# Kernel optimization log

Hardware: AMD Instinct MI355X
Metric: run time of the kernel (lower is better)

Reference implementation:

```python
import jax, jax.numpy as jnp
import numpy as np

EPS_NORM = 1e-12  # F.normalize eps
LN_EPS = 1e-5


def _ln(x, g, b):
    mu = x.mean(-1, keepdims=True)
    var = ((x - mu) ** 2).mean(-1, keepdims=True)
    return (x - mu) / jnp.sqrt(var + LN_EPS) * g + b


def _gate(x, w1, b1, g, b, w2, b2):
    # Linear -> LayerNorm(32) -> SiLU -> Linear -> Sigmoid, squeeze(-1)
    t = _ln(x @ w1 + b1, g, b)
    t = jax.nn.silu(t)
    return jax.nn.sigmoid(t @ w2 + b2)[..., 0]


def setup_inputs() -> dict:
    key = jax.random.key(0)
    B, N, D, dH, S, HID = 4, 4096, 1024, 256, 256, 32
    ks = jax.random.split(key, 24)
    sc_d = 0.5 * (6.0 / (D + dH)) ** 0.5  # xavier gain=0.5 approx
    sc_h = 0.5 * (6.0 / (D + HID)) ** 0.5
    inp = {
        "h": jax.random.normal(ks[0], (B, N, D), jnp.float32),
        # encoder complex projection (stored as (in,out))
        "Wr": jax.random.uniform(ks[1], (D, dH), jnp.float32, -sc_d, sc_d),
        "br": jnp.zeros((dH,), jnp.float32),
        "Wi": jax.random.uniform(ks[2], (D, dH), jnp.float32, -sc_d, sc_d),
        "bi": jnp.zeros((dH,), jnp.float32),
        # uncertainty net
        "uw1": jax.random.uniform(ks[3], (D, HID), jnp.float32, -sc_h, sc_h),
        "ub1": jnp.zeros((HID,), jnp.float32),
        "ug": jnp.ones((HID,), jnp.float32),
        "ubeta": jnp.zeros((HID,), jnp.float32),
        "uw2": jax.random.uniform(ks[4], (HID, 1), jnp.float32, -0.2, 0.2),
        "ub2": jnp.zeros((1,), jnp.float32),
        # decoherence gamma net
        "gw1": jax.random.uniform(ks[5], (D, HID), jnp.float32, -sc_h, sc_h),
        "gb1": jnp.zeros((HID,), jnp.float32),
        "gg": jnp.ones((HID,), jnp.float32),
        "gbeta": jnp.zeros((HID,), jnp.float32),
        "gw2": jax.random.uniform(ks[6], (HID, 1), jnp.float32, -0.2, 0.2),
        "gb2": jnp.zeros((1,), jnp.float32),
        # memory attention params
        "m_real": jax.random.normal(ks[7], (S, dH), jnp.float32) / dH ** 0.5,
        "m_imag": jax.random.normal(ks[8], (S, dH), jnp.float32) / dH ** 0.5,
        "values": jax.random.normal(ks[9], (S, D), jnp.float32) * 0.02,
        "ow": jax.random.uniform(ks[10], (D, D), jnp.float32, -0.5 * (3.0 / D) ** 0.5, 0.5 * (3.0 / D) ** 0.5),
        "ob": jnp.zeros((D,), jnp.float32),
        # norms
        "n1g": jnp.ones((D,), jnp.float32),
        "n1b": jnp.zeros((D,), jnp.float32),
        "n2g": jnp.ones((D,), jnp.float32),
        "n2b": jnp.zeros((D,), jnp.float32),
        # FFN
        "fw1": jax.random.normal(ks[11], (D, 4 * D), jnp.float32) * (2.0 / (5 * D)) ** 0.5,
        "fb1": jnp.zeros((4 * D,), jnp.float32),
        "fw2": jax.random.normal(ks[12], (4 * D, D), jnp.float32) * (2.0 / (5 * D)) ** 0.5,
        "fb2": jnp.zeros((D,), jnp.float32),
    }
    return inp


def reference(h, Wr, br, Wi, bi,
              uw1, ub1, ug, ubeta, uw2, ub2,
              gw1, gb1, gg, gbeta, gw2, gb2,
              m_real, m_imag, values, ow, ob,
              n1g, n1b, n2g, n2b, fw1, fb1, fw2, fb2):
    dH = m_real.shape[-1]
    # --- QuantumStateEncoder: psi = normalize(complex(Wr h, Wi h)), p in [0,0.95]
    pr = h @ Wr + br                       # (B,N,dH) real part
    pi = h @ Wi + bi                       # (B,N,dH) imag part
    nrm = jnp.maximum(jnp.sqrt(jnp.sum(pr * pr + pi * pi, -1, keepdims=True)), EPS_NORM)
    pr, pi = pr / nrm, pi / nrm
    p_init = _gate(h, uw1, ub1, ug, ubeta, uw2, ub2) * 0.95   # (B,N)
    # --- ContextualDecoherenceLayer: ctx = mean over N (identical per token)
    ctx = h.mean(axis=1)                   # (B,D)
    gamma = _gate(ctx, gw1, gb1, gg, gbeta, gw2, gb2)          # (B,)
    p = p_init * (1.0 - gamma[:, None])    # (B,N)
    # --- ExternalQuantumMemoryAttention
    mnrm = jnp.maximum(jnp.sqrt(jnp.sum(m_real * m_real + m_imag * m_imag, -1, keepdims=True)), EPS_NORM)
    Mr, Mi = m_real / mnrm, m_imag / mnrm  # (S,dH)
    # <psi|m> = sum conj(psi)*m ; |.|^2 is re^2+im^2
    re = jnp.einsum('bnd,sd->bns', pr, Mr) + jnp.einsum('bnd,sd->bns', pi, Mi)
    im = jnp.einsum('bnd,sd->bns', pr, Mi) - jnp.einsum('bnd,sd->bns', pi, Mr)
    overlap = re * re + im * im            # (B,N,S)
    raw = (1.0 - p)[..., None] * overlap + (p / dH)[..., None]
    attn = raw / (raw.sum(-1, keepdims=True) + 1e-8)
    attn_out = jnp.einsum('bns,sd->bnd', attn, values) @ ow + ob
    # --- residual + LN + FFN (dropout = eval identity)
    h1 = _ln(h + attn_out, n1g, n1b)
    ff = jax.nn.gelu(h1 @ fw1 + fb1, approximate=False) @ fw2 + fb2
    return _ln(h1 + ff, n2g, n2b)
```

## Files before the change

kernel.cpp:

```cpp
#include <hip/hip_runtime.h>
#include <math.h>


#define B_ 4
#define N_ 4096
#define D_ 1024
#define DH_ 256
#define S_ 256
#define HID_ 32
#define M_ (B_ * N_)

typedef unsigned short u16;
typedef unsigned int u32;
typedef __attribute__((ext_vector_type(8))) short bfrag;
typedef __attribute__((ext_vector_type(4))) float ffrag;

__device__ __forceinline__ float b2f(u16 u) {
    return __uint_as_float(((unsigned)u) << 16);
}
__device__ __forceinline__ u16 f2b(float f) {
    unsigned u = __float_as_uint(f);
    return (u16)((u + 0x7FFFu + ((u >> 16) & 1u)) >> 16);
}
__device__ __forceinline__ float fast_erf(float x) {
    float ax = fabsf(x);
    float t = __builtin_amdgcn_rcpf(fmaf(0.3275911f, ax, 1.f));
    float p = t * fmaf(t, fmaf(t, fmaf(t, fmaf(t, 1.061405429f, -1.453152027f),
                                       1.421413741f), -0.284496736f),
                       0.254829592f);
    float e = __expf(-ax * ax);
    float y = fmaf(-p, e, 1.f);
    return copysignf(y, x);
}
__device__ __forceinline__ float gelu_fast(float x) {
    return 0.5f * x * (1.0f + fast_erf(x * 0.70710678118654752440f));
}
__device__ __forceinline__ float ldf(const void* p, size_t i, bool bf) {
    return bf ? b2f(((const u16*)p)[i]) : ((const float*)p)[i];
}
__device__ __forceinline__ bool detect_bf(const void* n1g) {
    return *(const unsigned*)n1g == 0x3F803F80u;
}
__device__ __forceinline__ void gload16(const void* g, void* lds) {
    __builtin_amdgcn_global_load_lds(
        (const __attribute__((address_space(1))) u32*)g,
        (__attribute__((address_space(3))) u32*)lds, 16, 0, 0);
}

__global__ void zero_kernel(float* __restrict__ p, int n) {
    int i = blockIdx.x * 256 + threadIdx.x;
    if (i < n) p[i] = 0.f;
}

__global__ __launch_bounds__(256)
void h2b_kernel(const void* __restrict__ h, u16* __restrict__ hB,
                const void* __restrict__ n1g) {
    const bool bf = detect_bf(n1g);
    const size_t i = ((size_t)blockIdx.x * 256 + threadIdx.x) * 8;
    if (bf) {
        *(uint4*)(hB + i) = *(const uint4*)((const u16*)h + i);
    } else {
        const float* hf = (const float*)h;
        float4 x = *(const float4*)(hf + i);
        float4 y = *(const float4*)(hf + i + 4);
        union { u16 u[8]; uint4 v; } pk;
        pk.u[0] = f2b(x.x); pk.u[1] = f2b(x.y);
        pk.u[2] = f2b(x.z); pk.u[3] = f2b(x.w);
        pk.u[4] = f2b(y.x); pk.u[5] = f2b(y.y);
        pk.u[6] = f2b(y.z); pk.u[7] = f2b(y.w);
        *(uint4*)(hB + i) = pk.v;
    }
}

__global__ void pack_bias_kernel(const void* __restrict__ br,
                                 const void* __restrict__ bi,
                                 void* __restrict__ brbi,
                                 const void* __restrict__ n1g) {
    const bool bf = detect_bf(n1g);
    const int t = threadIdx.x;
    if (bf) {
        ((u16*)brbi)[t]       = ((const u16*)br)[t];
        ((u16*)brbi)[256 + t] = ((const u16*)bi)[t];
    } else {
        ((float*)brbi)[t]       = ((const float*)br)[t];
        ((float*)brbi)[256 + t] = ((const float*)bi)[t];
    }
}

__global__ __launch_bounds__(256)
void transpose_w_kernel(const void* __restrict__ W, u16* __restrict__ WT,
                        int K, int N, const void* __restrict__ n1g) {
    const bool bf = detect_bf(n1g);
    __shared__ u16 t[64][65];
    const int n0 = blockIdx.x * 64, k0 = blockIdx.y * 64;
    const int a = threadIdx.x & 63, b = threadIdx.x >> 6;
#pragma unroll
    for (int r = 0; r < 16; ++r) {
        int k = b * 16 + r;
        t[k][a] = f2b(ldf(W, (size_t)(k0 + k) * N + n0 + a, bf));
    }
    __syncthreads();
#pragma unroll
    for (int r = 0; r < 16; ++r) {
        int n = b * 16 + r;
        WT[(size_t)(n0 + n) * K + k0 + a] = t[a][n];
    }
}

__global__ __launch_bounds__(256)
void ctx_sum_kernel(const u16* __restrict__ hB, float* __restrict__ ctx) {
    const int chunks = N_ / 128;
    const int b = blockIdx.x / chunks;
    const int ch = blockIdx.x % chunks;
    const int tid = threadIdx.x;
    const size_t base = ((size_t)b * N_ + (size_t)ch * 128) * D_;
    float a[4] = {0.f, 0.f, 0.f, 0.f};
    for (int r = 0; r < 128; ++r)
#pragma unroll
        for (int q = 0; q < 4; ++q)
            a[q] += b2f(hB[base + (size_t)r * D_ + q * 256 + tid]);
#pragma unroll
    for (int q = 0; q < 4; ++q)
        atomicAdd(&ctx[b * D_ + q * 256 + tid], a[q]);
}

__global__ __launch_bounds__(128)
void gamma_gate_kernel(const float* __restrict__ ctx,
                       const void* __restrict__ w1, const void* __restrict__ b1,
                       const void* __restrict__ g, const void* __restrict__ beta,
                       const void* __restrict__ w2, const void* __restrict__ b2,
                       float* __restrict__ out, const void* __restrict__ n1g) {
    const bool bf = detect_bf(n1g);
    const int row = blockIdx.x;
    const int tid = threadIdx.x;
    const int col = tid & 31;
    const int chunk = tid >> 5;
    const float xscale = 1.f / (float)N_;

    float acc = 0.f;
    for (int k = chunk * 256; k < chunk * 256 + 256; ++k)
        acc += ctx[(size_t)row * D_ + k] * xscale * ldf(w1, (size_t)k * HID_ + col, bf);

    __shared__ float part[4][HID_];
    __shared__ float s[HID_];
    __shared__ float mu_s, rstd_s;
    part[chunk][col] = acc;
    __syncthreads();
    if (tid < HID_)
        s[tid] = part[0][tid] + part[1][tid] + part[2][tid] + part[3][tid]
               + ldf(b1, tid, bf);
    __syncthreads();
    if (tid == 0) {
        float m = 0.f;
        for (int i = 0; i < HID_; ++i) m += s[i];
        m /= (float)HID_;
        float var = 0.f;
        for (int i = 0; i < HID_; ++i) { float dd = s[i] - m; var += dd * dd; }
        var /= (float)HID_;
        mu_s = m;
        rstd_s = rsqrtf(var + 1e-5f);
    }
    __syncthreads();
    if (tid < HID_) {
        float v = (s[tid] - mu_s) * rstd_s * ldf(g, tid, bf) + ldf(beta, tid, bf);
        v = v / (1.f + expf(-v));
        s[tid] = v * ldf(w2, tid, bf);
    }
    __syncthreads();
    if (tid == 0) {
        float z = 0.f;
        for (int i = 0; i < HID_; ++i) z += s[i];
        z += ldf(b2, 0, bf);
        out[row] = 1.f / (1.f + expf(-z));
    }
}

__global__ __launch_bounds__(128)
void p_gate_kernel(const u16* __restrict__ hB,
                   const void* __restrict__ w1, const void* __restrict__ b1,
                   const void* __restrict__ g, const void* __restrict__ beta,
                   const void* __restrict__ w2, const void* __restrict__ b2,
                   float* __restrict__ out, const void* __restrict__ n1g) {
    const bool bf = detect_bf(n1g);
    const int row = blockIdx.x;
    const int tid = threadIdx.x;
    const int col = tid & 31;
    const int chunk = tid >> 5;

    float acc = 0.f;
    for (int k = chunk * 256; k < chunk * 256 + 256; ++k)
        acc += b2f(hB[(size_t)row * D_ + k]) * ldf(w1, (size_t)k * HID_ + col, bf);

    __shared__ float part[4][HID_];
    __shared__ float s[HID_];
    __shared__ float mu_s, rstd_s;
    part[chunk][col] = acc;
    __syncthreads();
    if (tid < HID_)
        s[tid] = part[0][tid] + part[1][tid] + part[2][tid] + part[3][tid]
               + ldf(b1, tid, bf);
    __syncthreads();
    if (tid == 0) {
        float m = 0.f;
        for (int i = 0; i < HID_; ++i) m += s[i];
        m /= (float)HID_;
        float var = 0.f;
        for (int i = 0; i < HID_; ++i) { float dd = s[i] - m; var += dd * dd; }
        var /= (float)HID_;
        mu_s = m;
        rstd_s = rsqrtf(var + 1e-5f);
    }
    __syncthreads();
    if (tid < HID_) {
        float v = (s[tid] - mu_s) * rstd_s * ldf(g, tid, bf) + ldf(beta, tid, bf);
        v = v / (1.f + expf(-v));
        s[tid] = v * ldf(w2, tid, bf);
    }
    __syncthreads();
    if (tid == 0) {
        float z = 0.f;
        for (int i = 0; i < HID_; ++i) z += s[i];
        z += ldf(b2, 0, bf);
        out[row] = 0.95f / (1.f + expf(-z));
    }
}

__global__ __launch_bounds__(256)
void norm_m_kernel(const void* __restrict__ m_real, const void* __restrict__ m_imag,
                   u16* __restrict__ bcatT, const void* __restrict__ n1g) {
    const bool bf = detect_bf(n1g);
    const int s = blockIdx.x;
    const int d = threadIdx.x;
    float mr = ldf(m_real, (size_t)s * DH_ + d, bf);
    float mi = ldf(m_imag, (size_t)s * DH_ + d, bf);
    float v = mr * mr + mi * mi;
#pragma unroll
    for (int off = 32; off; off >>= 1) v += __shfl_down(v, off, 64);
    __shared__ float red[4];
    if ((d & 63) == 0) red[d >> 6] = v;
    __syncthreads();
    float tot = red[0] + red[1] + red[2] + red[3];
    float inv = 1.f / fmaxf(sqrtf(tot), 1e-12f);
    float nr = mr * inv, ni = mi * inv;
    bcatT[(size_t)s * 512 + d]               = f2b(nr);
    bcatT[(size_t)s * 512 + 256 + d]         = f2b(ni);
    bcatT[(size_t)(256 + s) * 512 + d]       = f2b(ni);
    bcatT[(size_t)(256 + s) * 512 + 256 + d] = f2b(-nr);
}

__global__ __launch_bounds__(256)
void gemm_mfma(const u16* __restrict__ A, const u16* __restrict__ WT,
               const void* __restrict__ bias, void* __restrict__ out,
               int kseg, int lda, int ldw, int ldo,
               int act, int fo32, const void* __restrict__ n1g) {
    const bool bf = detect_bf(n1g);
    __shared__ short As[128 * 64];
    __shared__ short Bs[128 * 64];
    const int tid = threadIdx.x;

    const int nwg = gridDim.x * gridDim.y;
    const int flat = blockIdx.y * gridDim.x + blockIdx.x;
    const int xcd = flat & 7, idx = flat >> 3;
    const int qq = nwg >> 3, rr = nwg & 7;
    const int nf = (xcd < rr ? xcd * (qq + 1) : rr * (qq + 1) + (xcd - rr) * qq) + idx;
    const int c0 = (nf % gridDim.x) * 128;
    const int r0 = (nf / gridDim.x) * 128;

    const int lane = tid & 63, wave = tid >> 6;
    const int wm = wave & 1, wn = wave >> 1;
    const int quad = lane >> 4, l15 = lane & 15;
    const int l8 = lane >> 3;
    const int lc = (lane & 7) ^ l8;
    const int sx = l15 & 7;

    ffrag acc[4][4];
#pragma unroll
    for (int i = 0; i < 4; ++i)
#pragma unroll
        for (int j = 0; j < 4; ++j)
            acc[i][j] = (ffrag){0.f, 0.f, 0.f, 0.f};

    for (int k0 = 0; k0 < kseg; k0 += 64) {
        __syncthreads();
#pragma unroll
        for (int i = 0; i < 4; ++i) {
            int rb = wave * 32 + i * 8;
            gload16(A + (size_t)(r0 + rb + l8) * lda + k0 + lc * 8, &As[rb * 64]);
        }
#pragma unroll
        for (int i = 0; i < 4; ++i) {
            int rb = wave * 32 + i * 8;
            gload16(WT + (size_t)(c0 + rb + l8) * ldw + k0 + lc * 8, &Bs[rb * 64]);
        }
        __syncthreads();

#pragma unroll
        for (int ks = 0; ks < 2; ++ks) {
            bfrag a[4], b[4];
#pragma unroll
            for (int i = 0; i < 4; ++i) {
                int row = wm * 64 + i * 16 + l15;
                a[i] = *(const bfrag*)&As[row * 64 + (((ks * 4 + quad) ^ sx) * 8)];
            }
#pragma unroll
            for (int j = 0; j < 4; ++j) {
                int row = wn * 64 + j * 16 + l15;
                b[j] = *(const bfrag*)&Bs[row * 64 + (((ks * 4 + quad) ^ sx) * 8)];
            }
#pragma unroll
            for (int i = 0; i < 4; ++i)
#pragma unroll
                for (int j = 0; j < 4; ++j)
                    acc[i][j] = __builtin_amdgcn_mfma_f32_16x16x32_bf16(
                        a[i], b[j], acc[i][j], 0, 0, 0);
        }
    }

    float bv[4];
#pragma unroll
    for (int j = 0; j < 4; ++j)
        bv[j] = bias ? ldf(bias, c0 + wn * 64 + j * 16 + l15, bf) : 0.f;
#pragma unroll
    for (int i = 0; i < 4; ++i)
#pragma unroll
        for (int r = 0; r < 4; ++r) {
            int row_g = r0 + wm * 64 + i * 16 + quad * 4 + r;
#pragma unroll
            for (int j = 0; j < 4; ++j) {
                int col_g = c0 + wn * 64 + j * 16 + l15;
                float v = acc[i][j][r] + bv[j];
                if (act) v = gelu_fast(v);
                if (fo32) ((float*)out)[(size_t)row_g * ldo + col_g] = v;
                else      ((u16*)out)[(size_t)row_g * ldo + col_g] = f2b(v);
            }
        }
}

__global__ __launch_bounds__(512, 2)
void gemm_mfma2(const u16* __restrict__ A, const u16* __restrict__ WT,
                const void* __restrict__ bias, void* __restrict__ out,
                int K, int lda, int ldw, int ldo,
                int act, int fo32, const void* __restrict__ n1g) {
    const bool bf = detect_bf(n1g);
    __shared__ short As[2][256 * 64];
    __shared__ short Bs[2][256 * 64];
    const int tid = threadIdx.x;

    const int nwg = gridDim.x * gridDim.y;
    const int flat = blockIdx.y * gridDim.x + blockIdx.x;
    const int xcd = flat & 7, idx = flat >> 3;
    const int qq = nwg >> 3, rr = nwg & 7;
    const int nf = (xcd < rr ? xcd * (qq + 1) : rr * (qq + 1) + (xcd - rr) * qq) + idx;
    const int c0 = (nf % gridDim.x) * 256;
    const int r0 = (nf / gridDim.x) * 256;

    const int lane = tid & 63, wave = tid >> 6;
    const int wm = wave & 1, wn = wave >> 1;
    const int quad = lane >> 4, l15 = lane & 15;
    const int l8 = lane >> 3;
    const int lc = (lane & 7) ^ l8;
    const int sx = l15 & 7;

    ffrag acc[8][4];
#pragma unroll
    for (int i = 0; i < 8; ++i)
#pragma unroll
        for (int j = 0; j < 4; ++j)
            acc[i][j] = (ffrag){0.f, 0.f, 0.f, 0.f};

    auto STAGE_PIECE = [&](int buf, int k0, int pc) {
        int rb = pc * 64 + wave * 8;
        gload16(A + (size_t)(r0 + rb + l8) * lda + k0 + lc * 8,
                &As[buf][rb * 64]);
        gload16(WT + (size_t)(c0 + rb + l8) * ldw + k0 + lc * 8,
                &Bs[buf][rb * 64]);
    };

    bfrag a[8], b[4];
    auto PHASE_DS = [&](int buf, int ks) {
#pragma unroll
        for (int j = 0; j < 4; ++j) {
            int row = wn * 64 + j * 16 + l15;
            b[j] = *(const bfrag*)&Bs[buf][row * 64 + (((ks * 4 + quad) ^ sx) * 8)];
        }
#pragma unroll
        for (int i = 0; i < 8; ++i) {
            int row = wm * 128 + i * 16 + l15;
            a[i] = *(const bfrag*)&As[buf][row * 64 + (((ks * 4 + quad) ^ sx) * 8)];
        }
    };
    auto PHASE_MFMA = [&]() {
#pragma unroll
        for (int i = 0; i < 8; ++i)
#pragma unroll
            for (int j = 0; j < 4; ++j)
                acc[i][j] = __builtin_amdgcn_mfma_f32_16x16x32_bf16(
                    a[i], b[j], acc[i][j], 0, 0, 0);
    };

    const int nt = K >> 6;
#pragma unroll
    for (int pc = 0; pc < 4; ++pc) STAGE_PIECE(0, 0, pc);
    int cur = 0;
    for (int t = 0; t < nt; ++t) {
        const int kn = (t + 1) << 6;
        const bool pre = (t + 1 < nt);
        if (pre) {
            STAGE_PIECE(cur ^ 1, kn, 0);
            STAGE_PIECE(cur ^ 1, kn, 1);
            asm volatile("s_waitcnt vmcnt(4)" ::: "memory");
        } else {
            asm volatile("s_waitcnt vmcnt(0)" ::: "memory");
        }
        __builtin_amdgcn_s_barrier();
        PHASE_DS(cur, 0);
        asm volatile("s_waitcnt lgkmcnt(0)" ::: "memory");
        __builtin_amdgcn_sched_barrier(0);
        __builtin_amdgcn_s_setprio(1);
        PHASE_MFMA();
        __builtin_amdgcn_s_setprio(0);
        __builtin_amdgcn_sched_barrier(0);
        PHASE_DS(cur, 1);
        if (pre) {
            STAGE_PIECE(cur ^ 1, kn, 2);
            STAGE_PIECE(cur ^ 1, kn, 3);
        }
        __builtin_amdgcn_s_barrier();
        asm volatile("s_waitcnt lgkmcnt(0)" ::: "memory");
        __builtin_amdgcn_sched_barrier(0);
        __builtin_amdgcn_s_setprio(1);
        PHASE_MFMA();
        __builtin_amdgcn_s_setprio(0);
        __builtin_amdgcn_sched_barrier(0);
        __builtin_amdgcn_s_barrier();
        cur ^= 1;
    }

    float bv[4];
#pragma unroll
    for (int j = 0; j < 4; ++j)
        bv[j] = bias ? ldf(bias, c0 + wn * 64 + j * 16 + l15, bf) : 0.f;
#pragma unroll
    for (int i = 0; i < 8; ++i)
#pragma unroll
        for (int r = 0; r < 4; ++r) {
            int row_g = r0 + wm * 128 + i * 16 + quad * 4 + r;
#pragma unroll
            for (int j = 0; j < 4; ++j) {
                int col_g = c0 + wn * 64 + j * 16 + l15;
                float v = acc[i][j][r] + bv[j];
                if (act) v = gelu_fast(v);
                if (fo32) ((float*)out)[(size_t)row_g * ldo + col_g] = v;
                else      ((u16*)out)[(size_t)row_g * ldo + col_g] = f2b(v);
            }
        }
}

#define TPW 8
__global__ __launch_bounds__(256)
void attn_weights_kernel(const u16* __restrict__ psi,
                         const float* __restrict__ reim,
                         const float* __restrict__ p_init,
                         const float* __restrict__ gamma,
                         u16* __restrict__ a2) {
    const int token0 = blockIdx.x * TPW;
    const int tid = threadIdx.x;
    __shared__ float red[4];

    for (int tt = 0; tt < TPW; ++tt) {
        const size_t t = (size_t)(token0 + tt);
        float x0 = b2f(psi[t * 512 + tid]);
        float x1 = b2f(psi[t * 512 + 256 + tid]);
        float v = x0 * x0 + x1 * x1;
#pragma unroll
        for (int off = 32; off; off >>= 1) v += __shfl_down(v, off, 64);
        if ((tid & 63) == 0) red[tid >> 6] = v;
        __syncthreads();
        float inv = 1.f / fmaxf(red[0] + red[1] + red[2] + red[3], 1e-24f);

        float p = p_init[t] * (1.f - gamma[t / N_]);
        float re = reim[t * 512 + tid];
        float im = reim[t * 512 + 256 + tid];
        float raw = (1.f - p) * (re * re + im * im) * inv + p * (1.f / (float)DH_);

        float w = raw;
#pragma unroll
        for (int off = 32; off; off >>= 1) w += __shfl_down(w, off, 64);
        __syncthreads();
        if ((tid & 63) == 0) red[tid >> 6] = w;
        __syncthreads();
        float denom = red[0] + red[1] + red[2] + red[3];
        a2[t * 256 + tid] = f2b(raw / (denom + 1e-8f));
        __syncthreads();
    }
}

__global__ __launch_bounds__(256)
void copy_rows_kernel(const u16* __restrict__ src, u16* __restrict__ dst) {
    const int row = blockIdx.x;
    const int tid = threadIdx.x;
#pragma unroll
    for (int q = 0; q < 4; ++q)
        dst[(size_t)row * D_ + q * 256 + tid] = src[(size_t)row * D_ + q * 256 + tid];
}

__global__ __launch_bounds__(256)
void ln_add_kernel(const void* __restrict__ x, int xmode, size_t xrow0,
                   const void* __restrict__ y, int ymode,
                   const void* __restrict__ g, const void* __restrict__ b,
                   u16* __restrict__ outB, float* __restrict__ outF,
                   const void* __restrict__ n1g) {
    const bool bfin = detect_bf(n1g);
    const bool bfx = (xmode == 1) ? true : bfin;
    const int row = blockIdx.x;
    const int tid = threadIdx.x;
    __shared__ float red[4];

    float v[4];
#pragma unroll
    for (int q = 0; q < 4; ++q) {
        int d = q * 256 + tid;
        float yv = ymode ? ((const float*)y)[(size_t)row * D_ + d]
                         : b2f(((const u16*)y)[(size_t)row * D_ + d]);
        v[q] = ldf(x, (xrow0 + row) * (size_t)D_ + d, bfx) + yv;
    }

    float s = v[0] + v[1] + v[2] + v[3];
#pragma unroll
    for (int off = 32; off; off >>= 1) s += __shfl_down(s, off, 64);
    if ((tid & 63) == 0) red[tid >> 6] = s;
    __syncthreads();
    float mu = (red[0] + red[1] + red[2] + red[3]) * (1.f / (float)D_);
    __syncthreads();

    float q2 = 0.f;
#pragma unroll
    for (int j = 0; j < 4; ++j) { float dd = v[j] - mu; q2 += dd * dd; }
#pragma unroll
    for (int off = 32; off; off >>= 1) q2 += __shfl_down(q2, off, 64);
    if ((tid & 63) == 0) red[tid >> 6] = q2;
    __syncthreads();
    float var = (red[0] + red[1] + red[2] + red[3]) * (1.f / (float)D_);
    float rstd = rsqrtf(var + 1e-5f);

#pragma unroll
    for (int q = 0; q < 4; ++q) {
        int d = q * 256 + tid;
        float o = (v[q] - mu) * rstd * ldf(g, d, bfin) + ldf(b, d, bfin);
        if (outF) outF[(size_t)row * D_ + d] = o;
        else      outB[(size_t)row * D_ + d] = f2b(o);
    }
}

extern "C" void kernel_launch(void* const* d_in, const int* in_sizes, int n_in,
                              void* d_out, int out_size, void* d_ws, size_t ws_size,
                              hipStream_t stream) {
    const void* h      = d_in[0];
    const void* Wr     = d_in[1];
    const void* br     = d_in[2];
    const void* Wi     = d_in[3];
    const void* bi     = d_in[4];
    const void* uw1    = d_in[5];
    const void* ub1    = d_in[6];
    const void* ug     = d_in[7];
    const void* ubeta  = d_in[8];
    const void* uw2    = d_in[9];
    const void* ub2    = d_in[10];
    const void* gw1    = d_in[11];
    const void* gb1    = d_in[12];
    const void* gg     = d_in[13];
    const void* gbeta  = d_in[14];
    const void* gw2    = d_in[15];
    const void* gb2    = d_in[16];
    const void* m_real = d_in[17];
    const void* m_imag = d_in[18];
    const void* values = d_in[19];
    const void* ow     = d_in[20];
    const void* ob     = d_in[21];
    const void* n1g    = d_in[22];
    const void* n1b    = d_in[23];
    const void* n2g    = d_in[24];
    const void* n2b    = d_in[25];
    const void* fw1    = d_in[26];
    const void* fb1    = d_in[27];
    const void* fw2    = d_in[28];
    const void* fb2    = d_in[29];

    char*  ws      = (char*)d_ws;
    float* ctx     = (float*)(ws);
    float* gammap  = (float*)(ws + 16384);
    float* p_init  = (float*)(ws + 16448);
    void*  brbi    = (void*)(ws + 81984);
    u16*   BCatT   = (u16*)(ws + 84032);
    u16*   WrT     = (u16*)(ws + 608320);
    u16*   WiT     = (u16*)(ws + 1132608);
    u16*   owT     = (u16*)(ws + 2181184);
    u16*   fw1T    = (u16*)(ws + 4278336);
    u16*   fw2T    = (u16*)(ws + 12666944);
    const size_t tbase = 21055552;

    int CH = 16384;
    while (CH > 256 && tbase + (size_t)CH * 12288 > ws_size) CH >>= 1;
    u16*   t_buf = (u16*)(ws + tbase);
    float* pf    = (float*)(t_buf + (size_t)CH * 4096);

    float* outF    = (float*)d_out;
    u16*   Psi     = (u16*)d_out;
    u16*   A2      = Psi + (size_t)M_ * 512;
    u16*   VOT     = A2 + (size_t)M_ * 256;
    u16*   valuesB = VOT + (size_t)D_ * S_;
    u16*   X2      = (u16*)d_out + (size_t)M_ * D_;
    u16*   hB      = X2;
    float* REIMf   = (float*)X2;

    h2b_kernel<<<M_ * D_ / 2048, 256, 0, stream>>>(h, hB, n1g);
    h2b_kernel<<<S_ * D_ / 2048, 256, 0, stream>>>(values, valuesB, n1g);

    transpose_w_kernel<<<dim3(DH_ / 64, D_ / 64), 256, 0, stream>>>(Wr, WrT, D_, DH_, n1g);
    transpose_w_kernel<<<dim3(DH_ / 64, D_ / 64), 256, 0, stream>>>(Wi, WiT, D_, DH_, n1g);
    transpose_w_kernel<<<dim3(D_ / 64, D_ / 64), 256, 0, stream>>>(ow, owT, D_, D_, n1g);
    transpose_w_kernel<<<dim3(4 * D_ / 64, D_ / 64), 256, 0, stream>>>(fw1, fw1T, D_, 4 * D_, n1g);
    transpose_w_kernel<<<dim3(D_ / 64, 4 * D_ / 64), 256, 0, stream>>>(fw2, fw2T, 4 * D_, D_, n1g);
    pack_bias_kernel<<<1, 256, 0, stream>>>(br, bi, brbi, n1g);

    gemm_mfma<<<dim3(S_ / 128, D_ / 128), 256, 0, stream>>>(
        owT, valuesB, nullptr, VOT, D_, D_, D_, S_, 0, 0, n1g);

    zero_kernel<<<16, 256, 0, stream>>>(ctx, B_ * D_);
    ctx_sum_kernel<<<B_ * (N_ / 128), 256, 0, stream>>>(hB, ctx);
    gamma_gate_kernel<<<B_, 128, 0, stream>>>(ctx, gw1, gb1, gg, gbeta,
                                              gw2, gb2, gammap, n1g);

    norm_m_kernel<<<S_, 256, 0, stream>>>(m_real, m_imag, BCatT, n1g);

    gemm_mfma<<<dim3(512 / 128, M_ / 128), 256, 0, stream>>>(
        hB, WrT, brbi, Psi, D_, D_, D_, 512, 0, 0, n1g);

    p_gate_kernel<<<M_, 128, 0, stream>>>(hB, uw1, ub1, ug, ubeta,
                                          uw2, ub2, p_init, n1g);

    gemm_mfma<<<dim3(512 / 128, M_ / 128), 256, 0, stream>>>(
        Psi, BCatT, nullptr, REIMf, 512, 512, 512, 512, 0, 1, n1g);

    attn_weights_kernel<<<M_ / TPW, 256, 0, stream>>>(Psi, REIMf, p_init,
                                                      gammap, A2);

    for (int c = 0; c < M_ / CH; ++c) {
        const size_t offh = (size_t)c * CH * D_;
        gemm_mfma2<<<dim3(D_ / 256, CH / 256), 512, 0, stream>>>(
            A2 + (size_t)c * CH * S_, VOT, ob, pf, S_, S_, S_, D_, 0, 1, n1g);
        ln_add_kernel<<<CH, 256, 0, stream>>>(h, 0, (size_t)c * CH, pf, 1,
                                              n1g, n1b, X2 + offh, nullptr, n1g);
    }

    for (int c = 0; c < M_ / CH; ++c) {
        const size_t off = (size_t)c * CH * D_;
        gemm_mfma2<<<dim3(4 * D_ / 256, CH / 256), 512, 0, stream>>>(
            X2 + off, fw1T, fb1, t_buf, D_, D_, D_, 4 * D_, 1, 0, n1g);
        gemm_mfma2<<<dim3(D_ / 256, CH / 256), 512, 0, stream>>>(
            t_buf, fw2T, fb2, pf, 4 * D_, 4 * D_, 4 * D_, D_, 0, 1, n1g);
        copy_rows_kernel<<<CH, 256, 0, stream>>>(X2 + off, t_buf);
        ln_add_kernel<<<CH, 256, 0, stream>>>(t_buf, 1, 0, pf, 1,
                                              n2g, n2b, nullptr, outF + off, n1g);
    }
}
```

Measured before the change: 961.6 us.

## Switch GEMM to 32x32x16 MFMA tiles and vectorize context sum loads

The main GEMM's per-wave 128x64 tile moves from 16x16x32 bf16 MFMA fragments to 32x32x16 MFMA fragments. The LDS fragment reads, swizzle indexing and epilogue row/column mapping are redone to match the 32x32 accumulator layout. The intent is fewer LDS reads per FLOP and larger MFMA instructions with better throughput per issue. The ctx sum kernel also switches to 16-byte vector loads of 8 bf16 values per thread, with two row phases per block. The new epilogue store pattern writes 32 consecutive columns per row and may coalesce differently.

```diff
diff --git a/kernel.cpp b/kernel.cpp
--- a/kernel.cpp
+++ b/kernel.cpp
@@ -14,6 +14,7 @@
 typedef unsigned int u32;
 typedef __attribute__((ext_vector_type(8))) short bfrag;
 typedef __attribute__((ext_vector_type(4))) float ffrag;
+typedef __attribute__((ext_vector_type(16))) float ffrag16;
 
 __device__ __forceinline__ float b2f(u16 u) {
     return __uint_as_float(((unsigned)u) << 16);
@@ -113,15 +114,19 @@
     const int b = blockIdx.x / chunks;
     const int ch = blockIdx.x % chunks;
     const int tid = threadIdx.x;
+    const int colg = (tid & 127) * 8;
+    const int rp = tid >> 7;
     const size_t base = ((size_t)b * N_ + (size_t)ch * 128) * D_;
-    float a[4] = {0.f, 0.f, 0.f, 0.f};
-    for (int r = 0; r < 128; ++r)
-#pragma unroll
-        for (int q = 0; q < 4; ++q)
-            a[q] += b2f(hB[base + (size_t)r * D_ + q * 256 + tid]);
-#pragma unroll
-    for (int q = 0; q < 4; ++q)
-        atomicAdd(&ctx[b * D_ + q * 256 + tid], a[q]);
+    float a[8] = {};
+    for (int r = rp; r < 128; r += 2) {
+        uint4 v = *(const uint4*)(hB + base + (size_t)r * D_ + colg);
+        const u16* u = (const u16*)&v;
+#pragma unroll
+        for (int q = 0; q < 8; ++q) a[q] += b2f(u[q]);
+    }
+#pragma unroll
+    for (int q = 0; q < 8; ++q)
+        atomicAdd(&ctx[b * D_ + colg + q], a[q]);
 }
 
 __global__ __launch_bounds__(128)
@@ -356,17 +361,16 @@
 
     const int lane = tid & 63, wave = tid >> 6;
     const int wm = wave & 1, wn = wave >> 1;
-    const int quad = lane >> 4, l15 = lane & 15;
+    const int l31 = lane & 31, lh = lane >> 5;
     const int l8 = lane >> 3;
     const int lc = (lane & 7) ^ l8;
-    const int sx = l15 & 7;
-
-    ffrag acc[8][4];
-#pragma unroll
-    for (int i = 0; i < 8; ++i)
-#pragma unroll
-        for (int j = 0; j < 4; ++j)
-            acc[i][j] = (ffrag){0.f, 0.f, 0.f, 0.f};
+
+    ffrag16 acc[4][2];
+#pragma unroll
+    for (int i = 0; i < 4; ++i)
+#pragma unroll
+        for (int j = 0; j < 2; ++j)
+            acc[i][j] = (ffrag16)(0.f);
 
     auto STAGE_PIECE = [&](int buf, int k0, int pc) {
         int rb = pc * 64 + wave * 8;
@@ -376,26 +380,34 @@
                 &Bs[buf][rb * 64]);
     };
 
-    bfrag a[8], b[4];
-    auto PHASE_DS = [&](int buf, int ks) {
-#pragma unroll
-        for (int j = 0; j < 4; ++j) {
-            int row = wn * 64 + j * 16 + l15;
-            b[j] = *(const bfrag*)&Bs[buf][row * 64 + (((ks * 4 + quad) ^ sx) * 8)];
-        }
-#pragma unroll
-        for (int i = 0; i < 8; ++i) {
-            int row = wm * 128 + i * 16 + l15;
-            a[i] = *(const bfrag*)&As[buf][row * 64 + (((ks * 4 + quad) ^ sx) * 8)];
+    bfrag a[4][2], b[2][2];
+    auto PHASE_DS = [&](int buf, int ph) {
+#pragma unroll
+        for (int s = 0; s < 2; ++s) {
+            const int ksl = ph * 2 + s;
+#pragma unroll
+            for (int j = 0; j < 2; ++j) {
+                int row = wn * 64 + j * 32 + l31;
+                int chn = (ksl * 2 + lh) ^ (row & 7);
+                b[j][s] = *(const bfrag*)&Bs[buf][row * 64 + chn * 8];
+            }
+#pragma unroll
+            for (int i = 0; i < 4; ++i) {
+                int row = wm * 128 + i * 32 + l31;
+                int chn = (ksl * 2 + lh) ^ (row & 7);
+                a[i][s] = *(const bfrag*)&As[buf][row * 64 + chn * 8];
+            }
         }
     };
     auto PHASE_MFMA = [&]() {
 #pragma unroll
-        for (int i = 0; i < 8; ++i)
-#pragma unroll
-            for (int j = 0; j < 4; ++j)
-                acc[i][j] = __builtin_amdgcn_mfma_f32_16x16x32_bf16(
-                    a[i], b[j], acc[i][j], 0, 0, 0);
+        for (int s = 0; s < 2; ++s)
+#pragma unroll
+            for (int i = 0; i < 4; ++i)
+#pragma unroll
+                for (int j = 0; j < 2; ++j)
+                    acc[i][j] = __builtin_amdgcn_mfma_f32_32x32x16_bf16(
+                        a[i][s], b[j][s], acc[i][j], 0, 0, 0);
     };
 
     const int nt = K >> 6;
@@ -436,18 +448,18 @@
         cur ^= 1;
     }
 
-    float bv[4];
-#pragma unroll
-    for (int j = 0; j < 4; ++j)
-        bv[j] = bias ? ldf(bias, c0 + wn * 64 + j * 16 + l15, bf) : 0.f;
-#pragma unroll
-    for (int i = 0; i < 8; ++i)
-#pragma unroll
-        for (int r = 0; r < 4; ++r) {
-            int row_g = r0 + wm * 128 + i * 16 + quad * 4 + r;
-#pragma unroll
-            for (int j = 0; j < 4; ++j) {
-                int col_g = c0 + wn * 64 + j * 16 + l15;
+    float bv[2];
+#pragma unroll
+    for (int j = 0; j < 2; ++j)
+        bv[j] = bias ? ldf(bias, c0 + wn * 64 + j * 32 + l31, bf) : 0.f;
+#pragma unroll
+    for (int i = 0; i < 4; ++i)
+#pragma unroll
+        for (int r = 0; r < 16; ++r) {
+            int row_g = r0 + wm * 128 + i * 32 + (r & 3) + 8 * (r >> 2) + 4 * lh;
+#pragma unroll
+            for (int j = 0; j < 2; ++j) {
+                int col_g = c0 + wn * 64 + j * 32 + l31;
                 float v = acc[i][j][r] + bv[j];
                 if (act) v = gelu_fast(v);
                 if (fo32) ((float*)out)[(size_t)row_g * ldo + col_g] = v;
```

Result: slower. 1.002 ms (+4.3%).
